# Kernel optimization log

Hardware: AMD Instinct MI355X
Metric: run time of the kernel (lower is better)

The kernel has to match this reference:

```python
import jax, jax.numpy as jnp
import numpy as np

N_NODES = 100000
N_EDGES = 3200000
IN_DIM = 256
OUT_DIM = 128


def setup_inputs() -> dict:
    key = jax.random.key(0)
    k1, k2, k3, k4, k5 = jax.random.split(key, 5)
    # node features
    x = jax.random.normal(k1, (N_NODES, IN_DIM), dtype=jnp.float32)
    # glorot-uniform weight as in glorot_init
    init_range = np.sqrt(6.0 / (IN_DIM + OUT_DIM)).astype(np.float32)
    weight = jax.random.uniform(k2, (IN_DIM, OUT_DIM), dtype=jnp.float32,
                                minval=-init_range, maxval=init_range)
    # sparse adjacency in COO form: adj[dst, src] = edge_weight
    edge_src = jax.random.randint(k3, (N_EDGES,), 0, N_NODES, dtype=jnp.int64)
    edge_dst = jax.random.randint(k4, (N_EDGES,), 0, N_NODES, dtype=jnp.int64)
    edge_weight = jax.random.uniform(k5, (N_EDGES,), dtype=jnp.float32)
    return {"x": x, "weight": weight, "edge_weight": edge_weight,
            "edge_src": edge_src, "edge_dst": edge_dst}


def reference(x, weight, edge_weight, edge_src, edge_dst):
    # dense feature transform: [N, in] @ [in, out] -> [N, out]
    xw = x @ weight
    # sparse adjacency matmul (adj @ xw) as gather + weighted scatter-add
    msgs = xw[edge_src] * edge_weight[:, None]           # [E, out]
    agg = jax.ops.segment_sum(msgs, edge_dst, num_segments=N_NODES)
    # fused activation
    return jax.nn.relu(agg)
```

## Files before the change

kernel.cpp:

```cpp
#include <hip/hip_runtime.h>

#define IN_DIM 256
#define OUT_DIM 128
#define BM 64
#define BKG 64

#define BSHIFT 7
#define BNODES 128
#define MAXB2 832
#define CHUNK1 3584
#define CAPB 4736
#define HCAP 2560

typedef __attribute__((ext_vector_type(4))) float floatx4;
typedef __attribute__((ext_vector_type(8))) short shortx8;

static __device__ __forceinline__ unsigned short f2bf(float f) {
  unsigned u = __float_as_uint(f);
  u += 0x7FFFu + ((u >> 16) & 1u);
  return (unsigned short)(u >> 16);
}

__global__ __launch_bounds__(256) void prep_wt_kernel(
    const float* __restrict__ w, unsigned short* __restrict__ wt) {
  const int idx = blockIdx.x * 256 + threadIdx.x;
  const int k = idx >> 7;
  const int n = idx & 127;
  wt[n * IN_DIM + k] = f2bf(w[idx]);
}

__global__ __launch_bounds__(256) void gemm_xw_kernel(
    const float* __restrict__ x, const unsigned short* __restrict__ wt,
    unsigned short* __restrict__ xw, int n_nodes) {
  __shared__ unsigned short As[BM][BKG + 8];
  __shared__ unsigned short Bs[OUT_DIM][BKG + 8];

  const int t = threadIdx.x;
  const int wv = t >> 6;
  const int lane = t & 63;
  const int quad = lane >> 4;
  const int l16 = lane & 15;
  const int row0 = blockIdx.x * BM;
  if (row0 >= n_nodes) return;

  floatx4 acc[4][2];
#pragma unroll
  for (int a = 0; a < 4; ++a)
#pragma unroll
    for (int b = 0; b < 2; ++b) acc[a][b] = (floatx4){0.f, 0.f, 0.f, 0.f};

  for (int k0 = 0; k0 < IN_DIM; k0 += BKG) {
    __syncthreads();
#pragma unroll
    for (int i = 0; i < 4; ++i) {
      const int idx = i * 256 + t;
      const int r = idx >> 4;
      const int kq = (idx & 15) * 4;
      int row = row0 + r;
      if (row >= n_nodes) row = n_nodes - 1;
      const float4 v = *(const float4*)(x + (size_t)row * IN_DIM + k0 + kq);
      ushort4 sv;
      sv.x = f2bf(v.x); sv.y = f2bf(v.y); sv.z = f2bf(v.z); sv.w = f2bf(v.w);
      *(ushort4*)&As[r][kq] = sv;
    }
#pragma unroll
    for (int i = 0; i < 4; ++i) {
      const int idx16 = i * 256 + t;
      const int n = idx16 >> 3;
      const int off = (idx16 & 7) * 8;
      *(int4*)&Bs[n][off] = *(const int4*)(wt + (size_t)n * IN_DIM + k0 + off);
    }
    __syncthreads();

#pragma unroll
    for (int kk = 0; kk < BKG; kk += 32) {
      shortx8 af[4];
#pragma unroll
      for (int tm = 0; tm < 4; ++tm)
        af[tm] = *(const shortx8*)&As[tm * 16 + l16][kk + quad * 8];
      shortx8 bfr[2];
#pragma unroll
      for (int tn = 0; tn < 2; ++tn)
        bfr[tn] = *(const shortx8*)&Bs[wv * 32 + tn * 16 + l16][kk + quad * 8];
#pragma unroll
      for (int tm = 0; tm < 4; ++tm)
#pragma unroll
        for (int tn = 0; tn < 2; ++tn)
          acc[tm][tn] = __builtin_amdgcn_mfma_f32_16x16x32_bf16(
              af[tm], bfr[tn], acc[tm][tn], 0, 0, 0);
    }
  }

#pragma unroll
  for (int tm = 0; tm < 4; ++tm)
#pragma unroll
    for (int tn = 0; tn < 2; ++tn)
#pragma unroll
      for (int r = 0; r < 4; ++r) {
        const int grow = row0 + tm * 16 + quad * 4 + r;
        const int gcol = wv * 32 + tn * 16 + l16;
        if (grow < n_nodes)
          xw[(size_t)grow * OUT_DIM + gcol] = f2bf(acc[tm][tn][r]);
      }
}

__global__ __launch_bounds__(256) void partition_kernel(
    const int* __restrict__ esrc, const int* __restrict__ edst,
    const float* __restrict__ ew, int* __restrict__ btail,
    uint2* __restrict__ csr2, int n_edges, int nb2) {
  __shared__ uint2 srec[CHUNK1];
  __shared__ int hcnt[MAXB2];
  __shared__ int aux[MAXB2];
  __shared__ int sh[256];
  const int t = threadIdx.x;
  const int base = blockIdx.x * CHUNK1;
  const int cn = min(CHUNK1, n_edges - base);

  for (int b = t; b < MAXB2; b += 256) hcnt[b] = 0;
  __syncthreads();

  int dst[14];
  unsigned xpk[14];
#pragma unroll
  for (int i = 0; i < 14; ++i) {
    const int idx = t + i * 256;
    if (idx < cn) {
      const int e = base + idx;
      dst[i] = edst[e];
      unsigned wb = __float_as_uint(ew[e]);
      wb += 0x7FFFu + ((wb >> 16) & 1u);
      xpk[i] = ((wb >> 16) << 17) | (unsigned)esrc[e];
      atomicAdd(&hcnt[((unsigned)dst[i]) >> BSHIFT], 1);
    } else {
      dst[i] = -1;
    }
  }
  __syncthreads();
  {
    const int b4 = 4 * t;
    int a0 = 0, a1 = 0, a2 = 0, a3 = 0;
    if (b4 < MAXB2) {
      a0 = hcnt[b4]; a1 = hcnt[b4 + 1]; a2 = hcnt[b4 + 2]; a3 = hcnt[b4 + 3];
    }
    const int s = a0 + a1 + a2 + a3;
    sh[t] = s;
    __syncthreads();
    for (int off = 1; off < 256; off <<= 1) {
      const int add = (t >= off) ? sh[t - off] : 0;
      __syncthreads();
      sh[t] += add;
      __syncthreads();
    }
    if (b4 < MAXB2) {
      int run = sh[t] - s;
      aux[b4] = run; run += a0;
      aux[b4 + 1] = run; run += a1;
      aux[b4 + 2] = run; run += a2;
      aux[b4 + 3] = run;
    }
  }
  __syncthreads();
  for (int b = t; b < nb2; b += 256) {
    const int c = hcnt[b];
    const int lo = aux[b];
    int g = 0;
    if (c) g = b * CAPB + atomicAdd(&btail[b], c);
    hcnt[b] = lo;
    aux[b] = g - lo;
  }
  __syncthreads();
#pragma unroll
  for (int i = 0; i < 14; ++i)
    if (dst[i] >= 0) {
      const int bk = ((unsigned)dst[i]) >> BSHIFT;
      const int p = atomicAdd(&hcnt[bk], 1);
      srec[p] = make_uint2(xpk[i], (unsigned)dst[i]);
    }
  __syncthreads();
  for (int i = t; i < cn; i += 256) {
    const uint2 r = srec[i];
    const int bk = r.y >> BSHIFT;
    const size_t pos = (size_t)(aux[bk] + i);
    if (pos < (size_t)(bk + 1) * CAPB) csr2[pos] = r;
  }
}

struct AggSmem {
  unsigned xs[HCAP];
  int cnt[64];
  int cur[64];
  int sst[64];
  int sen[64];
  int sh[64];
};

__global__ __launch_bounds__(256) void sort_agg_kernel(
    const uint2* __restrict__ csr2, const int* __restrict__ btail,
    const unsigned short* __restrict__ xw, float* __restrict__ out,
    int n_nodes) {
  __shared__ __align__(16) AggSmem sm;
  const int t = threadIdx.x;
  const int bucket = blockIdx.x >> 1;
  const int half = blockIdx.x & 1;
  const int node0 = (bucket << BSHIFT) + half * 64;
  const size_t S = (size_t)bucket * CAPB;
  const int cnt = min(btail[bucket], CAPB);

  if (t < 64) sm.cnt[t] = 0;
  __syncthreads();
  for (int i = t; i < cnt; i += 256) {
    const unsigned y = csr2[S + i].y & (BNODES - 1);
    if ((int)(y >> 6) == half) atomicAdd(&sm.cnt[y & 63], 1);
  }
  __syncthreads();
  {
    const int s = (t < 64) ? sm.cnt[t] : 0;
    if (t < 64) sm.sh[t] = s;
    __syncthreads();
    for (int off = 1; off < 64; off <<= 1) {
      const int add = (t >= off && t < 64) ? sm.sh[t - off] : 0;
      __syncthreads();
      if (t < 64) sm.sh[t] += add;
      __syncthreads();
    }
    if (t < 64) {
      const int run = sm.sh[t] - s;
      sm.cur[t] = run;
      sm.sst[t] = run;
      sm.sen[t] = run + s;
    }
  }
  __syncthreads();
  for (int i = t; i < cnt; i += 256) {
    const uint2 r = csr2[S + i];
    const unsigned y = r.y & (BNODES - 1);
    if ((int)(y >> 6) == half) {
      const int p = atomicAdd(&sm.cur[y & 63], 1);
      if (p < HCAP) sm.xs[p] = r.x;
    }
  }
  __syncthreads();

  const int g = t >> 4;
  const int lane = t & 15;
  const int d8 = lane * 8;

  for (int nl = g; nl < 64; nl += 16) {
    const int node = node0 + nl;
    if (node >= n_nodes) continue;
    const int j0 = sm.sst[nl];
    const int j1 = min(sm.sen[nl], HCAP);

    float a0 = 0.f, a1 = 0.f, a2 = 0.f, a3 = 0.f;
    float a4 = 0.f, a5 = 0.f, a6 = 0.f, a7 = 0.f;
    float c0 = 0.f, c1 = 0.f, c2 = 0.f, c3 = 0.f;
    float c4 = 0.f, c5 = 0.f, c6 = 0.f, c7 = 0.f;

    int j = j0;
    for (; j + 4 <= j1; j += 4) {
      const unsigned p0 = sm.xs[j];
      const unsigned p1 = sm.xs[j + 1];
      const unsigned p2 = sm.xs[j + 2];
      const unsigned p3 = sm.xs[j + 3];
      const uint4 v0 = *(const uint4*)(xw + (size_t)(p0 & 0x1FFFFu) * OUT_DIM + d8);
      const uint4 v1 = *(const uint4*)(xw + (size_t)(p1 & 0x1FFFFu) * OUT_DIM + d8);
      const uint4 v2 = *(const uint4*)(xw + (size_t)(p2 & 0x1FFFFu) * OUT_DIM + d8);
      const uint4 v3 = *(const uint4*)(xw + (size_t)(p3 & 0x1FFFFu) * OUT_DIM + d8);
      const float w0 = __uint_as_float((p0 >> 17) << 16);
      const float w1 = __uint_as_float((p1 >> 17) << 16);
      const float w2 = __uint_as_float((p2 >> 17) << 16);
      const float w3 = __uint_as_float((p3 >> 17) << 16);
      a0 = fmaf(__uint_as_float(v0.x << 16), w0, a0);
      a1 = fmaf(__uint_as_float(v0.x & 0xFFFF0000u), w0, a1);
      a2 = fmaf(__uint_as_float(v0.y << 16), w0, a2);
      a3 = fmaf(__uint_as_float(v0.y & 0xFFFF0000u), w0, a3);
      a4 = fmaf(__uint_as_float(v0.z << 16), w0, a4);
      a5 = fmaf(__uint_as_float(v0.z & 0xFFFF0000u), w0, a5);
      a6 = fmaf(__uint_as_float(v0.w << 16), w0, a6);
      a7 = fmaf(__uint_as_float(v0.w & 0xFFFF0000u), w0, a7);
      c0 = fmaf(__uint_as_float(v1.x << 16), w1, c0);
      c1 = fmaf(__uint_as_float(v1.x & 0xFFFF0000u), w1, c1);
      c2 = fmaf(__uint_as_float(v1.y << 16), w1, c2);
      c3 = fmaf(__uint_as_float(v1.y & 0xFFFF0000u), w1, c3);
      c4 = fmaf(__uint_as_float(v1.z << 16), w1, c4);
      c5 = fmaf(__uint_as_float(v1.z & 0xFFFF0000u), w1, c5);
      c6 = fmaf(__uint_as_float(v1.w << 16), w1, c6);
      c7 = fmaf(__uint_as_float(v1.w & 0xFFFF0000u), w1, c7);
      a0 = fmaf(__uint_as_float(v2.x << 16), w2, a0);
      a1 = fmaf(__uint_as_float(v2.x & 0xFFFF0000u), w2, a1);
      a2 = fmaf(__uint_as_float(v2.y << 16), w2, a2);
      a3 = fmaf(__uint_as_float(v2.y & 0xFFFF0000u), w2, a3);
      a4 = fmaf(__uint_as_float(v2.z << 16), w2, a4);
      a5 = fmaf(__uint_as_float(v2.z & 0xFFFF0000u), w2, a5);
      a6 = fmaf(__uint_as_float(v2.w << 16), w2, a6);
      a7 = fmaf(__uint_as_float(v2.w & 0xFFFF0000u), w2, a7);
      c0 = fmaf(__uint_as_float(v3.x << 16), w3, c0);
      c1 = fmaf(__uint_as_float(v3.x & 0xFFFF0000u), w3, c1);
      c2 = fmaf(__uint_as_float(v3.y << 16), w3, c2);
      c3 = fmaf(__uint_as_float(v3.y & 0xFFFF0000u), w3, c3);
      c4 = fmaf(__uint_as_float(v3.z << 16), w3, c4);
      c5 = fmaf(__uint_as_float(v3.z & 0xFFFF0000u), w3, c5);
      c6 = fmaf(__uint_as_float(v3.w << 16), w3, c6);
      c7 = fmaf(__uint_as_float(v3.w & 0xFFFF0000u), w3, c7);
    }
    for (; j < j1; ++j) {
      const unsigned p0 = sm.xs[j];
      const float w0 = __uint_as_float((p0 >> 17) << 16);
      const uint4 v0 = *(const uint4*)(xw + (size_t)(p0 & 0x1FFFFu) * OUT_DIM + d8);
      a0 = fmaf(__uint_as_float(v0.x << 16), w0, a0);
      a1 = fmaf(__uint_as_float(v0.x & 0xFFFF0000u), w0, a1);
      a2 = fmaf(__uint_as_float(v0.y << 16), w0, a2);
      a3 = fmaf(__uint_as_float(v0.y & 0xFFFF0000u), w0, a3);
      a4 = fmaf(__uint_as_float(v0.z << 16), w0, a4);
      a5 = fmaf(__uint_as_float(v0.z & 0xFFFF0000u), w0, a5);
      a6 = fmaf(__uint_as_float(v0.w << 16), w0, a6);
      a7 = fmaf(__uint_as_float(v0.w & 0xFFFF0000u), w0, a7);
    }

    float4 o0, o1;
    o0.x = fmaxf(a0 + c0, 0.f); o0.y = fmaxf(a1 + c1, 0.f);
    o0.z = fmaxf(a2 + c2, 0.f); o0.w = fmaxf(a3 + c3, 0.f);
    o1.x = fmaxf(a4 + c4, 0.f); o1.y = fmaxf(a5 + c5, 0.f);
    o1.z = fmaxf(a6 + c6, 0.f); o1.w = fmaxf(a7 + c7, 0.f);
    float* orow = out + (size_t)node * OUT_DIM + d8;
    *(float4*)orow = o0;
    *(float4*)(orow + 4) = o1;
  }
}

extern "C" void kernel_launch(void* const* d_in, const int* in_sizes, int n_in,
                              void* d_out, int out_size, void* d_ws,
                              size_t ws_size, hipStream_t stream) {
  const float* x    = (const float*)d_in[0];
  const float* w    = (const float*)d_in[1];
  const float* ew   = (const float*)d_in[2];
  const int*   esrc = (const int*)d_in[3];
  const int*   edst = (const int*)d_in[4];
  float* out = (float*)d_out;

  const int n_edges = in_sizes[2];
  const int n_nodes = out_size / OUT_DIM;
  const int nb2 = (n_nodes + BNODES - 1) >> BSHIFT;

  char* p = (char*)d_ws;
  unsigned short* xw = (unsigned short*)p;
  p += (size_t)n_nodes * OUT_DIM * sizeof(unsigned short);
  p = (char*)(((uintptr_t)p + 15) & ~(uintptr_t)15);
  unsigned short* wt = (unsigned short*)p;
  p += (size_t)OUT_DIM * IN_DIM * sizeof(unsigned short);
  p = (char*)(((uintptr_t)p + 15) & ~(uintptr_t)15);
  uint2* csr2 = (uint2*)p;  p += (size_t)nb2 * CAPB * sizeof(uint2);
  int* btail = (int*)p;     p += (size_t)nb2 * sizeof(int);

  hipMemsetAsync(btail, 0, (size_t)nb2 * sizeof(int), stream);

  prep_wt_kernel<<<(IN_DIM * OUT_DIM) / 256, 256, 0, stream>>>(w, wt);

  const int pblocks = (n_edges + CHUNK1 - 1) / CHUNK1;
  partition_kernel<<<pblocks, 256, 0, stream>>>(esrc, edst, ew, btail, csr2,
                                                n_edges, nb2);

  gemm_xw_kernel<<<(n_nodes + BM - 1) / BM, 256, 0, stream>>>(x, wt, xw,
                                                              n_nodes);

  sort_agg_kernel<<<2 * nb2, 256, 0, stream>>>(csr2, btail, xw, out, n_nodes);
}
```

Measured before the change: 372.9 us.

## Fuse edge partition and GEMM into one interleaved launch, drop memset

Merges the edge-partitioning kernel and the bf16 MFMA GEMM into one launch. Blocks alternate between partition and GEMM roles, so the memory-bound scatter and the compute-bound matmul can share the GPU at the same time, and one launch plus its gap is removed. The btail memset moves into the weight-prep kernel. The aggregation loop now issues 8 gathers per iteration into a single accumulator set instead of 4 into two sets, and gets launch bounds asking for 8 blocks. The fused kernel's shared memory is a union sized by the larger partition layout, which may lower occupancy for the GEMM blocks.

```diff
diff --git a/kernel.cpp b/kernel.cpp
--- a/kernel.cpp
+++ b/kernel.cpp
@@ -21,167 +21,192 @@
   return (unsigned short)(u >> 16);
 }
 
-__global__ __launch_bounds__(256) void prep_wt_kernel(
-    const float* __restrict__ w, unsigned short* __restrict__ wt) {
+__global__ __launch_bounds__(256) void prep_kernel(
+    const float* __restrict__ w, unsigned short* __restrict__ wt,
+    int* __restrict__ btail, int nb2) {
   const int idx = blockIdx.x * 256 + threadIdx.x;
   const int k = idx >> 7;
   const int n = idx & 127;
   wt[n * IN_DIM + k] = f2bf(w[idx]);
-}
-
-__global__ __launch_bounds__(256) void gemm_xw_kernel(
+  if (blockIdx.x == 0)
+    for (int b = threadIdx.x; b < nb2; b += 256) btail[b] = 0;
+}
+
+__global__ __launch_bounds__(256) void fused_pg_kernel(
     const float* __restrict__ x, const unsigned short* __restrict__ wt,
-    unsigned short* __restrict__ xw, int n_nodes) {
-  __shared__ unsigned short As[BM][BKG + 8];
-  __shared__ unsigned short Bs[OUT_DIM][BKG + 8];
-
-  const int t = threadIdx.x;
-  const int wv = t >> 6;
-  const int lane = t & 63;
-  const int quad = lane >> 4;
-  const int l16 = lane & 15;
-  const int row0 = blockIdx.x * BM;
-  if (row0 >= n_nodes) return;
-
-  floatx4 acc[4][2];
-#pragma unroll
-  for (int a = 0; a < 4; ++a)
-#pragma unroll
-    for (int b = 0; b < 2; ++b) acc[a][b] = (floatx4){0.f, 0.f, 0.f, 0.f};
-
-  for (int k0 = 0; k0 < IN_DIM; k0 += BKG) {
-    __syncthreads();
-#pragma unroll
-    for (int i = 0; i < 4; ++i) {
-      const int idx = i * 256 + t;
-      const int r = idx >> 4;
-      const int kq = (idx & 15) * 4;
-      int row = row0 + r;
-      if (row >= n_nodes) row = n_nodes - 1;
-      const float4 v = *(const float4*)(x + (size_t)row * IN_DIM + k0 + kq);
-      ushort4 sv;
-      sv.x = f2bf(v.x); sv.y = f2bf(v.y); sv.z = f2bf(v.z); sv.w = f2bf(v.w);
-      *(ushort4*)&As[r][kq] = sv;
-    }
-#pragma unroll
-    for (int i = 0; i < 4; ++i) {
-      const int idx16 = i * 256 + t;
-      const int n = idx16 >> 3;
-      const int off = (idx16 & 7) * 8;
-      *(int4*)&Bs[n][off] = *(const int4*)(wt + (size_t)n * IN_DIM + k0 + off);
-    }
-    __syncthreads();
-
-#pragma unroll
-    for (int kk = 0; kk < BKG; kk += 32) {
-      shortx8 af[4];
-#pragma unroll
-      for (int tm = 0; tm < 4; ++tm)
-        af[tm] = *(const shortx8*)&As[tm * 16 + l16][kk + quad * 8];
-      shortx8 bfr[2];
-#pragma unroll
-      for (int tn = 0; tn < 2; ++tn)
-        bfr[tn] = *(const shortx8*)&Bs[wv * 32 + tn * 16 + l16][kk + quad * 8];
-#pragma unroll
-      for (int tm = 0; tm < 4; ++tm)
-#pragma unroll
-        for (int tn = 0; tn < 2; ++tn)
-          acc[tm][tn] = __builtin_amdgcn_mfma_f32_16x16x32_bf16(
-              af[tm], bfr[tn], acc[tm][tn], 0, 0, 0);
-    }
-  }
-
-#pragma unroll
-  for (int tm = 0; tm < 4; ++tm)
-#pragma unroll
-    for (int tn = 0; tn < 2; ++tn)
-#pragma unroll
-      for (int r = 0; r < 4; ++r) {
-        const int grow = row0 + tm * 16 + quad * 4 + r;
-        const int gcol = wv * 32 + tn * 16 + l16;
-        if (grow < n_nodes)
-          xw[(size_t)grow * OUT_DIM + gcol] = f2bf(acc[tm][tn][r]);
-      }
-}
-
-__global__ __launch_bounds__(256) void partition_kernel(
+    unsigned short* __restrict__ xw, int n_nodes,
     const int* __restrict__ esrc, const int* __restrict__ edst,
     const float* __restrict__ ew, int* __restrict__ btail,
-    uint2* __restrict__ csr2, int n_edges, int nb2) {
-  __shared__ uint2 srec[CHUNK1];
-  __shared__ int hcnt[MAXB2];
-  __shared__ int aux[MAXB2];
-  __shared__ int sh[256];
+    uint2* __restrict__ csr2, int n_edges, int nb2, int pblocks) {
+  __shared__ __align__(16) union {
+    struct {
+      unsigned short As[BM][BKG + 8];
+      unsigned short Bs[OUT_DIM][BKG + 8];
+    } g;
+    struct {
+      uint2 srec[CHUNK1];
+      int hcnt[MAXB2];
+      int aux[MAXB2];
+      int sh[256];
+    } p;
+  } sm;
+
+  const int bid = blockIdx.x;
+  const int P = pblocks;
+  const int G = (int)gridDim.x - pblocks;
+  bool is_part;
+  int vb;
+  if (P <= G) {
+    if (bid < 2 * P) { is_part = !(bid & 1); vb = bid >> 1; }
+    else             { is_part = false;      vb = bid - P; }
+  } else {
+    if (bid < 2 * G) { is_part = (bid & 1);  vb = bid >> 1; }
+    else             { is_part = true;       vb = bid - G; }
+  }
+
   const int t = threadIdx.x;
-  const int base = blockIdx.x * CHUNK1;
-  const int cn = min(CHUNK1, n_edges - base);
-
-  for (int b = t; b < MAXB2; b += 256) hcnt[b] = 0;
-  __syncthreads();
-
-  int dst[14];
-  unsigned xpk[14];
-#pragma unroll
-  for (int i = 0; i < 14; ++i) {
-    const int idx = t + i * 256;
-    if (idx < cn) {
-      const int e = base + idx;
-      dst[i] = edst[e];
-      unsigned wb = __float_as_uint(ew[e]);
-      wb += 0x7FFFu + ((wb >> 16) & 1u);
-      xpk[i] = ((wb >> 16) << 17) | (unsigned)esrc[e];
-      atomicAdd(&hcnt[((unsigned)dst[i]) >> BSHIFT], 1);
-    } else {
-      dst[i] = -1;
-    }
-  }
-  __syncthreads();
-  {
-    const int b4 = 4 * t;
-    int a0 = 0, a1 = 0, a2 = 0, a3 = 0;
-    if (b4 < MAXB2) {
-      a0 = hcnt[b4]; a1 = hcnt[b4 + 1]; a2 = hcnt[b4 + 2]; a3 = hcnt[b4 + 3];
-    }
-    const int s = a0 + a1 + a2 + a3;
-    sh[t] = s;
-    __syncthreads();
-    for (int off = 1; off < 256; off <<= 1) {
-      const int add = (t >= off) ? sh[t - off] : 0;
-      __syncthreads();
-      sh[t] += add;
-      __syncthreads();
-    }
-    if (b4 < MAXB2) {
-      int run = sh[t] - s;
-      aux[b4] = run; run += a0;
-      aux[b4 + 1] = run; run += a1;
-      aux[b4 + 2] = run; run += a2;
-      aux[b4 + 3] = run;
-    }
-  }
-  __syncthreads();
-  for (int b = t; b < nb2; b += 256) {
-    const int c = hcnt[b];
-    const int lo = aux[b];
-    int g = 0;
-    if (c) g = b * CAPB + atomicAdd(&btail[b], c);
-    hcnt[b] = lo;
-    aux[b] = g - lo;
-  }
-  __syncthreads();
-#pragma unroll
-  for (int i = 0; i < 14; ++i)
-    if (dst[i] >= 0) {
-      const int bk = ((unsigned)dst[i]) >> BSHIFT;
-      const int p = atomicAdd(&hcnt[bk], 1);
-      srec[p] = make_uint2(xpk[i], (unsigned)dst[i]);
-    }
-  __syncthreads();
-  for (int i = t; i < cn; i += 256) {
-    const uint2 r = srec[i];
-    const int bk = r.y >> BSHIFT;
-    const size_t pos = (size_t)(aux[bk] + i);
-    if (pos < (size_t)(bk + 1) * CAPB) csr2[pos] = r;
+
+  if (is_part) {
+    const int base = vb * CHUNK1;
+    const int cn = min(CHUNK1, n_edges - base);
+
+    for (int b = t; b < MAXB2; b += 256) sm.p.hcnt[b] = 0;
+    __syncthreads();
+
+    int dst[14];
+    unsigned xpk[14];
+#pragma unroll
+    for (int i = 0; i < 14; ++i) {
+      const int idx = t + i * 256;
+      if (idx < cn) {
+        const int e = base + idx;
+        dst[i] = edst[e];
+        unsigned wb = __float_as_uint(ew[e]);
+        wb += 0x7FFFu + ((wb >> 16) & 1u);
+        xpk[i] = ((wb >> 16) << 17) | (unsigned)esrc[e];
+        atomicAdd(&sm.p.hcnt[((unsigned)dst[i]) >> BSHIFT], 1);
+      } else {
+        dst[i] = -1;
+      }
+    }
+    __syncthreads();
+    {
+      const int b4 = 4 * t;
+      int a0 = 0, a1 = 0, a2 = 0, a3 = 0;
+      if (b4 < MAXB2) {
+        a0 = sm.p.hcnt[b4];     a1 = sm.p.hcnt[b4 + 1];
+        a2 = sm.p.hcnt[b4 + 2]; a3 = sm.p.hcnt[b4 + 3];
+      }
+      const int s = a0 + a1 + a2 + a3;
+      sm.p.sh[t] = s;
+      __syncthreads();
+      for (int off = 1; off < 256; off <<= 1) {
+        const int add = (t >= off) ? sm.p.sh[t - off] : 0;
+        __syncthreads();
+        sm.p.sh[t] += add;
+        __syncthreads();
+      }
+      if (b4 < MAXB2) {
+        int run = sm.p.sh[t] - s;
+        sm.p.aux[b4] = run; run += a0;
+        sm.p.aux[b4 + 1] = run; run += a1;
+        sm.p.aux[b4 + 2] = run; run += a2;
+        sm.p.aux[b4 + 3] = run;
+      }
+    }
+    __syncthreads();
+    for (int b = t; b < nb2; b += 256) {
+      const int c = sm.p.hcnt[b];
+      const int lo = sm.p.aux[b];
+      int g = 0;
+      if (c) g = b * CAPB + atomicAdd(&btail[b], c);
+      sm.p.hcnt[b] = lo;
+      sm.p.aux[b] = g - lo;
+    }
+    __syncthreads();
+#pragma unroll
+    for (int i = 0; i < 14; ++i)
+      if (dst[i] >= 0) {
+        const int bk = ((unsigned)dst[i]) >> BSHIFT;
+        const int p = atomicAdd(&sm.p.hcnt[bk], 1);
+        sm.p.srec[p] = make_uint2(xpk[i], (unsigned)dst[i]);
+      }
+    __syncthreads();
+    for (int i = t; i < cn; i += 256) {
+      const uint2 r = sm.p.srec[i];
+      const int bk = r.y >> BSHIFT;
+      const size_t pos = (size_t)(sm.p.aux[bk] + i);
+      if (pos < (size_t)(bk + 1) * CAPB) csr2[pos] = r;
+    }
+  } else {
+    const int wv = t >> 6;
+    const int lane = t & 63;
+    const int quad = lane >> 4;
+    const int l16 = lane & 15;
+    const int row0 = vb * BM;
+    if (row0 >= n_nodes) return;
+
+    floatx4 acc[4][2];
+#pragma unroll
+    for (int a = 0; a < 4; ++a)
+#pragma unroll
+      for (int b = 0; b < 2; ++b) acc[a][b] = (floatx4){0.f, 0.f, 0.f, 0.f};
+
+    for (int k0 = 0; k0 < IN_DIM; k0 += BKG) {
+      __syncthreads();
+#pragma unroll
+      for (int i = 0; i < 4; ++i) {
+        const int idx = i * 256 + t;
+        const int r = idx >> 4;
+        const int kq = (idx & 15) * 4;
+        int row = row0 + r;
+        if (row >= n_nodes) row = n_nodes - 1;
+        const float4 v = *(const float4*)(x + (size_t)row * IN_DIM + k0 + kq);
+        ushort4 sv;
+        sv.x = f2bf(v.x); sv.y = f2bf(v.y); sv.z = f2bf(v.z); sv.w = f2bf(v.w);
+        *(ushort4*)&sm.g.As[r][kq] = sv;
+      }
+#pragma unroll
+      for (int i = 0; i < 4; ++i) {
+        const int idx16 = i * 256 + t;
+        const int n = idx16 >> 3;
+        const int off = (idx16 & 7) * 8;
+        *(int4*)&sm.g.Bs[n][off] =
+            *(const int4*)(wt + (size_t)n * IN_DIM + k0 + off);
+      }
+      __syncthreads();
+
+#pragma unroll
+      for (int kk = 0; kk < BKG; kk += 32) {
+        shortx8 af[4];
+#pragma unroll
+        for (int tm = 0; tm < 4; ++tm)
+          af[tm] = *(const shortx8*)&sm.g.As[tm * 16 + l16][kk + quad * 8];
+        shortx8 bfr[2];
+#pragma unroll
+        for (int tn = 0; tn < 2; ++tn)
+          bfr[tn] =
+              *(const shortx8*)&sm.g.Bs[wv * 32 + tn * 16 + l16][kk + quad * 8];
+#pragma unroll
+        for (int tm = 0; tm < 4; ++tm)
+#pragma unroll
+          for (int tn = 0; tn < 2; ++tn)
+            acc[tm][tn] = __builtin_amdgcn_mfma_f32_16x16x32_bf16(
+                af[tm], bfr[tn], acc[tm][tn], 0, 0, 0);
+      }
+    }
+
+#pragma unroll
+    for (int tm = 0; tm < 4; ++tm)
+#pragma unroll
+      for (int tn = 0; tn < 2; ++tn)
+#pragma unroll
+        for (int r = 0; r < 4; ++r) {
+          const int grow = row0 + tm * 16 + quad * 4 + r;
+          const int gcol = wv * 32 + tn * 16 + l16;
+          if (grow < n_nodes)
+            xw[(size_t)grow * OUT_DIM + gcol] = f2bf(acc[tm][tn][r]);
+        }
   }
 }
 
@@ -194,7 +219,7 @@
   int sh[64];
 };
 
-__global__ __launch_bounds__(256) void sort_agg_kernel(
+__global__ __launch_bounds__(256, 8) void sort_agg_kernel(
     const uint2* __restrict__ csr2, const int* __restrict__ btail,
     const unsigned short* __restrict__ xw, float* __restrict__ out,
     int n_nodes) {
@@ -244,6 +269,7 @@
   const int g = t >> 4;
   const int lane = t & 15;
   const int d8 = lane * 8;
+  const unsigned short* __restrict__ xwd = xw + d8;
 
   for (int nl = g; nl < 64; nl += 16) {
     const int node = node0 + nl;
@@ -253,23 +279,33 @@
 
     float a0 = 0.f, a1 = 0.f, a2 = 0.f, a3 = 0.f;
     float a4 = 0.f, a5 = 0.f, a6 = 0.f, a7 = 0.f;
-    float c0 = 0.f, c1 = 0.f, c2 = 0.f, c3 = 0.f;
-    float c4 = 0.f, c5 = 0.f, c6 = 0.f, c7 = 0.f;
 
     int j = j0;
-    for (; j + 4 <= j1; j += 4) {
+    for (; j + 8 <= j1; j += 8) {
+      uint4 v[8];
+      float wq[8];
+#pragma unroll
+      for (int u = 0; u < 8; ++u) {
+        const unsigned p = sm.xs[j + u];
+        v[u] = *(const uint4*)(xwd + (size_t)(p & 0x1FFFFu) * OUT_DIM);
+        wq[u] = __uint_as_float((p >> 17) << 16);
+      }
+#pragma unroll
+      for (int u = 0; u < 8; ++u) {
+        a0 = fmaf(__uint_as_float(v[u].x << 16), wq[u], a0);
+        a1 = fmaf(__uint_as_float(v[u].x & 0xFFFF0000u), wq[u], a1);
+        a2 = fmaf(__uint_as_float(v[u].y << 16), wq[u], a2);
+        a3 = fmaf(__uint_as_float(v[u].y & 0xFFFF0000u), wq[u], a3);
+        a4 = fmaf(__uint_as_float(v[u].z << 16), wq[u], a4);
+        a5 = fmaf(__uint_as_float(v[u].z & 0xFFFF0000u), wq[u], a5);
+        a6 = fmaf(__uint_as_float(v[u].w << 16), wq[u], a6);
+        a7 = fmaf(__uint_as_float(v[u].w & 0xFFFF0000u), wq[u], a7);
+      }
+    }
+    for (; j < j1; ++j) {
       const unsigned p0 = sm.xs[j];
-      const unsigned p1 = sm.xs[j + 1];
-      const unsigned p2 = sm.xs[j + 2];
-      const unsigned p3 = sm.xs[j + 3];
-      const uint4 v0 = *(const uint4*)(xw + (size_t)(p0 & 0x1FFFFu) * OUT_DIM + d8);
-      const uint4 v1 = *(const uint4*)(xw + (size_t)(p1 & 0x1FFFFu) * OUT_DIM + d8);
-      const uint4 v2 = *(const uint4*)(xw + (size_t)(p2 & 0x1FFFFu) * OUT_DIM + d8);
-      const uint4 v3 = *(const uint4*)(xw + (size_t)(p3 & 0x1FFFFu) * OUT_DIM + d8);
       const float w0 = __uint_as_float((p0 >> 17) << 16);
-      const float w1 = __uint_as_float((p1 >> 17) << 16);
-      const float w2 = __uint_as_float((p2 >> 17) << 16);
-      const float w3 = __uint_as_float((p3 >> 17) << 16);
+      const uint4 v0 = *(const uint4*)(xwd + (size_t)(p0 & 0x1FFFFu) * OUT_DIM);
       a0 = fmaf(__uint_as_float(v0.x << 16), w0, a0);
       a1 = fmaf(__uint_as_float(v0.x & 0xFFFF0000u), w0, a1);
       a2 = fmaf(__uint_as_float(v0.y << 16), w0, a2);
@@ -278,50 +314,13 @@
       a5 = fmaf(__uint_as_float(v0.z & 0xFFFF0000u), w0, a5);
       a6 = fmaf(__uint_as_float(v0.w << 16), w0, a6);
       a7 = fmaf(__uint_as_float(v0.w & 0xFFFF0000u), w0, a7);
-      c0 = fmaf(__uint_as_float(v1.x << 16), w1, c0);
-      c1 = fmaf(__uint_as_float(v1.x & 0xFFFF0000u), w1, c1);
-      c2 = fmaf(__uint_as_float(v1.y << 16), w1, c2);
-      c3 = fmaf(__uint_as_float(v1.y & 0xFFFF0000u), w1, c3);
-      c4 = fmaf(__uint_as_float(v1.z << 16), w1, c4);
-      c5 = fmaf(__uint_as_float(v1.z & 0xFFFF0000u), w1, c5);
-      c6 = fmaf(__uint_as_float(v1.w << 16), w1, c6);
-      c7 = fmaf(__uint_as_float(v1.w & 0xFFFF0000u), w1, c7);
-      a0 = fmaf(__uint_as_float(v2.x << 16), w2, a0);
-      a1 = fmaf(__uint_as_float(v2.x & 0xFFFF0000u), w2, a1);
-      a2 = fmaf(__uint_as_float(v2.y << 16), w2, a2);
-      a3 = fmaf(__uint_as_float(v2.y & 0xFFFF0000u), w2, a3);
-      a4 = fmaf(__uint_as_float(v2.z << 16), w2, a4);
-      a5 = fmaf(__uint_as_float(v2.z & 0xFFFF0000u), w2, a5);
-      a6 = fmaf(__uint_as_float(v2.w << 16), w2, a6);
-      a7 = fmaf(__uint_as_float(v2.w & 0xFFFF0000u), w2, a7);
-      c0 = fmaf(__uint_as_float(v3.x << 16), w3, c0);
-      c1 = fmaf(__uint_as_float(v3.x & 0xFFFF0000u), w3, c1);
-      c2 = fmaf(__uint_as_float(v3.y << 16), w3, c2);
-      c3 = fmaf(__uint_as_float(v3.y & 0xFFFF0000u), w3, c3);
-      c4 = fmaf(__uint_as_float(v3.z << 16), w3, c4);
-      c5 = fmaf(__uint_as_float(v3.z & 0xFFFF0000u), w3, c5);
-      c6 = fmaf(__uint_as_float(v3.w << 16), w3, c6);
-      c7 = fmaf(__uint_as_float(v3.w & 0xFFFF0000u), w3, c7);
-    }
-    for (; j < j1; ++j) {
-      const unsigned p0 = sm.xs[j];
-      const float w0 = __uint_as_float((p0 >> 17) << 16);
-      const uint4 v0 = *(const uint4*)(xw + (size_t)(p0 & 0x1FFFFu) * OUT_DIM + d8);
-      a0 = fmaf(__uint_as_float(v0.x << 16), w0, a0);
-      a1 = fmaf(__uint_as_float(v0.x & 0xFFFF0000u), w0, a1);
-      a2 = fmaf(__uint_as_float(v0.y << 16), w0, a2);
-      a3 = fmaf(__uint_as_float(v0.y & 0xFFFF0000u), w0, a3);
-      a4 = fmaf(__uint_as_float(v0.z << 16), w0, a4);
-      a5 = fmaf(__uint_as_float(v0.z & 0xFFFF0000u), w0, a5);
-      a6 = fmaf(__uint_as_float(v0.w << 16), w0, a6);
-      a7 = fmaf(__uint_as_float(v0.w & 0xFFFF0000u), w0, a7);
     }
 
     float4 o0, o1;
-    o0.x = fmaxf(a0 + c0, 0.f); o0.y = fmaxf(a1 + c1, 0.f);
-    o0.z = fmaxf(a2 + c2, 0.f); o0.w = fmaxf(a3 + c3, 0.f);
-    o1.x = fmaxf(a4 + c4, 0.f); o1.y = fmaxf(a5 + c5, 0.f);
-    o1.z = fmaxf(a6 + c6, 0.f); o1.w = fmaxf(a7 + c7, 0.f);
+    o0.x = fmaxf(a0, 0.f); o0.y = fmaxf(a1, 0.f);
+    o0.z = fmaxf(a2, 0.f); o0.w = fmaxf(a3, 0.f);
+    o1.x = fmaxf(a4, 0.f); o1.y = fmaxf(a5, 0.f);
+    o1.z = fmaxf(a6, 0.f); o1.w = fmaxf(a7, 0.f);
     float* orow = out + (size_t)node * OUT_DIM + d8;
     *(float4*)orow = o0;
     *(float4*)(orow + 4) = o1;
@@ -352,16 +351,12 @@
   uint2* csr2 = (uint2*)p;  p += (size_t)nb2 * CAPB * sizeof(uint2);
   int* btail = (int*)p;     p += (size_t)nb2 * sizeof(int);
 
-  hipMemsetAsync(btail, 0, (size_t)nb2 * sizeof(int), stream);
-
-  prep_wt_kernel<<<(IN_DIM * OUT_DIM) / 256, 256, 0, stream>>>(w, wt);
+  prep_kernel<<<(IN_DIM * OUT_DIM) / 256, 256, 0, stream>>>(w, wt, btail, nb2);
 
   const int pblocks = (n_edges + CHUNK1 - 1) / CHUNK1;
-  partition_kernel<<<pblocks, 256, 0, stream>>>(esrc, edst, ew, btail, csr2,
-                                                n_edges, nb2);
-
-  gemm_xw_kernel<<<(n_nodes + BM - 1) / BM, 256, 0, stream>>>(x, wt, xw,
-                                                              n_nodes);
+  const int gblocks = (n_nodes + BM - 1) / BM;
+  fused_pg_kernel<<<pblocks + gblocks, 256, 0, stream>>>(
+      x, wt, xw, n_nodes, esrc, edst, ew, btail, csr2, n_edges, nb2, pblocks);
 
   sort_agg_kernel<<<2 * nb2, 256, 0, stream>>>(csr2, btail, xw, out, n_nodes);
 }
```

Measured after the change: 355.8 us. -4.6%, faster.
